# Kernel optimization log

Measured on AMD Instinct MI355X. Metric: run time of the kernel, lower is better.

## Reference

```python
import math
import jax, jax.numpy as jnp
import numpy as np

B, S, D, H, L, FF, V = 4, 512, 512, 8, 2, 2048, 32000
MAXSEQ = 1024
HD = D // H
SCALE = 1.0 / math.sqrt(HD)
EMB_SCALE = math.sqrt(D)


def _ln(x, w, b):
    m = x.mean(-1, keepdims=True)
    v = ((x - m) ** 2).mean(-1, keepdims=True)
    return (x - m) / jnp.sqrt(v + 1e-5) * w + b


def setup_inputs() -> dict:
    key = jax.random.key(0)
    ks = jax.random.split(key, 16)
    def n(i, shape):
        return 0.02 * jax.random.normal(ks[i], shape, dtype=jnp.float32)
    z = lambda shape: jnp.zeros(shape, dtype=jnp.float32)
    return {
        "input_ids": jax.random.randint(ks[0], (B, S), 0, V),
        "tok_emb": n(1, (V, D)),
        "pos_emb": n(2, (MAXSEQ, D)),
        "layer_weights": z((L + 1,)),
        "kW": n(3, (D, D)), "kb": z((D,)),
        "vW": n(4, (D, D)), "vb": z((D,)),
        "qW": n(5, (L, D, D)), "qb": z((L, D)),
        "oW": n(6, (L, D, D)), "ob": z((L, D)),
        "f1W": n(7, (L, D, FF)), "f1b": z((L, FF)),
        "f2W": n(8, (L, FF, D)), "f2b": z((L, D)),
        "ln1w": jnp.ones((L, D)), "ln1b": z((L, D)),
        "ln2w": jnp.ones((L, D)), "ln2b": z((L, D)),
        "lnfw": jnp.ones((D,)), "lnfb": z((D,)),
        "headW": n(9, (D, V)),
    }


def reference(input_ids, tok_emb, pos_emb, layer_weights, kW, kb, vW, vb,
              qW, qb, oW, ob, f1W, f1b, f2W, f2b,
              ln1w, ln1b, ln2w, ln2b, lnfw, lnfb, headW):
    # embeddings: (B,S,D)
    emb = tok_emb[input_ids] * EMB_SCALE + pos_emb[:S][None]
    w = jax.nn.softmax(layer_weights)  # (L+1,)

    def run_layers(x, mk, mv, mask):
        # x: (B,D); mk,mv: (B,M,D); mask: (M,) bool
        outs = [x]
        M = mk.shape[1]
        k = mk.reshape(B, M, H, HD)
        v = mv.reshape(B, M, H, HD)
        for l in range(L):
            q = (x @ qW[l] + qb[l]).reshape(B, H, HD)
            s = jnp.einsum('bhd,bmhd->bhm', q, k) * SCALE
            s = jnp.where(mask[None, None, :], s, -1e9)
            a = jax.nn.softmax(s, axis=-1)
            att = jnp.einsum('bhm,bmhd->bhd', a, v).reshape(B, D)
            att = att @ oW[l] + ob[l]
            x = _ln(x + att, ln1w[l], ln1b[l])
            ff = jax.nn.relu(x @ f1W[l] + f1b[l]) @ f2W[l] + f2b[l]
            x = _ln(x + ff, ln2w[l], ln2b[l])
            outs.append(x)
        return x, jnp.stack(outs, 0)  # (B,D), (L+1,B,D)

    # t = 0: no prior memory -> attend to K/V of the current embedding (mem_len=1)
    x0 = emb[:, 0]
    mk0 = (x0 @ kW + kb)[:, None, :]
    mv0 = (x0 @ vW + vb)[:, None, :]
    out0, louts0 = run_layers(x0, mk0, mv0, jnp.ones((1,), dtype=bool))
    m0 = jnp.einsum('l,lbd->bd', w, louts0)
    memk = jnp.zeros((B, S, D), dtype=emb.dtype).at[:, 0].set(m0 @ kW + kb)
    memv = jnp.zeros((B, S, D), dtype=emb.dtype).at[:, 0].set(m0 @ vW + vb)

    pos = jnp.arange(S)

    def step(carry, inputs):
        mk, mv = carry
        t, x = inputs  # t scalar int, x: (B,D)
        mask = pos < t  # valid memory slots: m_0..m_{t-1}
        out, louts = run_layers(x, mk, mv, mask)
        m = jnp.einsum('l,lbd->bd', w, louts)
        mk = mk.at[:, t].set(m @ kW + kb)
        mv = mv.at[:, t].set(m @ vW + vb)
        return (mk, mv), out

    ts = jnp.arange(1, S)
    xs_in = emb[:, 1:].transpose(1, 0, 2)  # (S-1,B,D)
    _, outs = jax.lax.scan(step, (memk, memv), (ts, xs_in))
    hidden = jnp.concatenate([out0[None], outs], axis=0).transpose(1, 0, 2)  # (B,S,D)
    hidden = _ln(hidden, lnfw, lnfb)
    return hidden @ headW  # (B,S,V)
```

## Files before the change

### kernel.cpp

```cpp
#include <hip/hip_runtime.h>
#include <hip/hip_cooperative_groups.h>
#include <math.h>

namespace cg = cooperative_groups;

#define NB 4
#define NS 512
#define ND 512
#define NH 8
#define NHD 64
#define NL 2
#define NFF 2048
#define NV 32000
#define ATT_SCALE 0.125f
#define EMB_SCALEF 22.627416997969522f

struct P {
  const int* ids;
  const float *tok, *pos, *lw, *kW, *kb, *vW, *vb, *qW, *qb, *oW, *ob;
  const float *f1W, *f1b, *f2W, *f2b, *ln1w, *ln1b, *ln2w, *ln2b, *lnfw, *lnfb, *headW;
  float *emb, *memk, *memv, *hidden, *q, *att, *r1, *r2, *ff1, *kv0k, *kv0v;
};

__device__ __forceinline__ float blk_sum(float v, float* red) {
  #pragma unroll
  for (int o = 32; o > 0; o >>= 1) v += __shfl_down(v, o, 64);
  const int tid = threadIdx.x;
  __syncthreads();
  if ((tid & 63) == 0) red[tid >> 6] = v;
  __syncthreads();
  return red[0] + red[1] + red[2] + red[3];
}

__device__ __forceinline__ float blk_max(float v, float* red) {
  #pragma unroll
  for (int o = 32; o > 0; o >>= 1) v = fmaxf(v, __shfl_down(v, o, 64));
  const int tid = threadIdx.x;
  __syncthreads();
  if ((tid & 63) == 0) red[tid >> 6] = v;
  __syncthreads();
  return fmaxf(fmaxf(red[0], red[1]), fmaxf(red[2], red[3]));
}

__device__ __forceinline__ void ln_stats(const float* __restrict__ v, float& mean, float& rstd, float* red) {
  const int tid = threadIdx.x;
  float s = 0.f, q = 0.f;
  for (int i = tid; i < ND; i += 256) { float x = v[i]; s += x; q += x * x; }
  s = blk_sum(s, red);
  q = blk_sum(q, red);
  mean = s * (1.0f / ND);
  rstd = rsqrtf(q * (1.0f / ND) - mean * mean + 1e-5f);
}

__global__ void __launch_bounds__(256) scan_kernel(P p) {
  cg::grid_group grid = cg::this_grid();
  const int wg = blockIdx.x;
  const int b = wg >> 4;
  const int sl = wg & 15;
  const int tid = threadIdx.x;

  __shared__ float xs[2048];
  __shared__ float part[256];
  __shared__ float red[4];

  for (int i = wg * 256 + tid; i < NB * NS * ND; i += 64 * 256) {
    int d = i & (ND - 1);
    int bs = i >> 9;
    int t = bs & (NS - 1);
    int bb = bs >> 9;
    p.emb[i] = p.tok[(size_t)p.ids[bb * NS + t] * ND + d] * EMB_SCALEF + p.pos[t * ND + d];
  }
  grid.sync();

  {
    for (int i = tid; i < ND; i += 256) xs[i] = p.emb[(size_t)b * NS * ND + i];
    __syncthreads();
    int oid = tid & 63, chunk = tid >> 6;
    bool isv = oid >= 32;
    int j = sl * 32 + (oid & 31);
    const float* W = isv ? p.vW : p.kW;
    const float* wp = W + (size_t)(chunk * 128) * ND + j;
    float acc = 0.f;
    #pragma unroll 4
    for (int d = 0; d < 128; d++) acc = fmaf(xs[chunk * 128 + d], wp[(size_t)d * ND], acc);
    part[tid] = acc;
    __syncthreads();
    if (tid < 64) {
      float r = part[tid] + part[64 + tid] + part[128 + tid] + part[192 + tid];
      bool iv = tid >= 32;
      int jj = sl * 32 + (tid & 31);
      if (!iv) p.kv0k[b * ND + jj] = r + p.kb[jj];
      else     p.kv0v[b * ND + jj] = r + p.vb[jj];
    }
  }
  grid.sync();

  float w0, w1, w2;
  {
    float a0 = p.lw[0], a1 = p.lw[1], a2 = p.lw[2];
    float mx = fmaxf(a0, fmaxf(a1, a2));
    float e0 = expf(a0 - mx), e1 = expf(a1 - mx), e2 = expf(a2 - mx);
    float inv = 1.f / (e0 + e1 + e2);
    w0 = e0 * inv; w1 = e1 * inv; w2 = e2 * inv;
  }

  for (int t = 0; t < NS; t++) {
    const float* xin0 = p.emb + ((size_t)b * NS + t) * ND;
    const int len = (t == 0) ? 1 : t;

    for (int l = 0; l < NL; l++) {
      if (l == 0) {
        for (int i = tid; i < ND; i += 256) xs[i] = xin0[i];
        __syncthreads();
      } else {
        const float* rv = p.r2 + (size_t)b * ND;
        float mean, rstd;
        ln_stats(rv, mean, rstd, red);
        for (int i = tid; i < ND; i += 256)
          xs[i] = (rv[i] - mean) * rstd * p.ln2w[i] + p.ln2b[i];
        __syncthreads();
      }
      {
        int jl = tid & 31, chunk = tid >> 5;
        int j = sl * 32 + jl;
        const float* wp = p.qW + (size_t)l * ND * ND + (size_t)(chunk * 64) * ND + j;
        float acc = 0.f;
        #pragma unroll 4
        for (int d = 0; d < 64; d++) acc = fmaf(xs[chunk * 64 + d], wp[(size_t)d * ND], acc);
        part[tid] = acc;
        __syncthreads();
        if (tid < 32) {
          float r = 0.f;
          #pragma unroll
          for (int c = 0; c < 8; c++) r += part[c * 32 + tid];
          int j2 = sl * 32 + tid;
          p.q[b * ND + j2] = r + p.qb[l * ND + j2];
        }
      }
      grid.sync();

      if (wg < 32) {
        int ab = wg >> 3, ah = wg & 7;
        const float* kp = (t == 0) ? (p.kv0k + ab * ND) : (p.memk + (size_t)ab * NS * ND);
        const float* vp = (t == 0) ? (p.kv0v + ab * ND) : (p.memv + (size_t)ab * NS * ND);
        if (tid < 64) xs[512 + tid] = p.q[ab * ND + ah * NHD + tid];
        __syncthreads();
        float lmax = -1e30f;
        for (int m = tid; m < len; m += 256) {
          const float* kr = kp + (size_t)m * ND + ah * NHD;
          float acc = 0.f;
          #pragma unroll
          for (int i = 0; i < NHD; i++) acc = fmaf(xs[512 + i], kr[i], acc);
          float sv = acc * ATT_SCALE;
          xs[m] = sv;
          lmax = fmaxf(lmax, sv);
        }
        lmax = blk_max(lmax, red);
        float lsum = 0.f;
        for (int m = tid; m < len; m += 256) { float e = expf(xs[m] - lmax); xs[m] = e; lsum += e; }
        lsum = blk_sum(lsum, red);
        float inv = 1.f / lsum;
        int hd = tid & 63, ch = tid >> 6;
        float acc = 0.f;
        for (int m = ch; m < len; m += 4) acc = fmaf(xs[m], vp[(size_t)m * ND + ah * NHD + hd], acc);
        part[tid] = acc;
        __syncthreads();
        if (tid < 64) {
          float r = (part[tid] + part[64 + tid] + part[128 + tid] + part[192 + tid]) * inv;
          p.att[ab * ND + ah * NHD + tid] = r;
        }
      }
      grid.sync();

      {
        for (int i = tid; i < ND; i += 256) xs[i] = p.att[b * ND + i];
        float mean = 0.f, rstd = 0.f;
        if (l == 1) {
          const float* rv = p.r2 + (size_t)b * ND;
          ln_stats(rv, mean, rstd, red);
        }
        __syncthreads();
        int jl = tid & 31, chunk = tid >> 5;
        int j = sl * 32 + jl;
        const float* wp = p.oW + (size_t)l * ND * ND + (size_t)(chunk * 64) * ND + j;
        float acc = 0.f;
        #pragma unroll 4
        for (int d = 0; d < 64; d++) acc = fmaf(xs[chunk * 64 + d], wp[(size_t)d * ND], acc);
        part[tid] = acc;
        __syncthreads();
        if (tid < 32) {
          float r = 0.f;
          #pragma unroll
          for (int c = 0; c < 8; c++) r += part[c * 32 + tid];
          int j2 = sl * 32 + tid;
          float xinv;
          if (l == 0) xinv = xin0[j2];
          else {
            const float* rv = p.r2 + (size_t)b * ND;
            xinv = (rv[j2] - mean) * rstd * p.ln2w[j2] + p.ln2b[j2];
          }
          p.r1[b * ND + j2] = xinv + r + p.ob[l * ND + j2];
        }
      }
      grid.sync();

      {
        const float* rv = p.r1 + b * ND;
        float mean, rstd;
        ln_stats(rv, mean, rstd, red);
        for (int i = tid; i < ND; i += 256)
          xs[i] = (rv[i] - mean) * rstd * p.ln1w[l * ND + i] + p.ln1b[l * ND + i];
        __syncthreads();
        int jl = tid & 127, chunk = tid >> 7;
        int j = sl * 128 + jl;
        const float* wp = p.f1W + (size_t)l * ND * NFF + (size_t)(chunk * 256) * NFF + j;
        float acc = 0.f;
        #pragma unroll 4
        for (int d = 0; d < 256; d++) acc = fmaf(xs[chunk * 256 + d], wp[(size_t)d * NFF], acc);
        part[tid] = acc;
        __syncthreads();
        if (tid < 128) {
          float r = part[tid] + part[128 + tid] + p.f1b[l * NFF + sl * 128 + tid];
          p.ff1[b * NFF + sl * 128 + tid] = fmaxf(r, 0.f);
        }
      }
      grid.sync();

      {
        for (int i = tid; i < NFF; i += 256) xs[i] = p.ff1[b * NFF + i];
        const float* rv = p.r1 + b * ND;
        float mean, rstd;
        ln_stats(rv, mean, rstd, red);
        __syncthreads();
        int jl = tid & 31, chunk = tid >> 5;
        int j = sl * 32 + jl;
        const float* wp = p.f2W + (size_t)l * NFF * ND + (size_t)(chunk * 256) * ND + j;
        float acc = 0.f;
        #pragma unroll 4
        for (int d = 0; d < 256; d++) acc = fmaf(xs[chunk * 256 + d], wp[(size_t)d * ND], acc);
        part[tid] = acc;
        __syncthreads();
        if (tid < 32) {
          float r = 0.f;
          #pragma unroll
          for (int c = 0; c < 8; c++) r += part[c * 32 + tid];
          int j2 = sl * 32 + tid;
          float x1 = (rv[j2] - mean) * rstd * p.ln1w[l * ND + j2] + p.ln1b[l * ND + j2];
          p.r2[((size_t)l * NB + b) * ND + j2] = x1 + r + p.f2b[l * ND + j2];
        }
      }
      grid.sync();
    }

    {
      const float* r20 = p.r2 + (size_t)b * ND;
      const float* r21 = p.r2 + ((size_t)NB + b) * ND;
      float m0, s0, m1, s1;
      ln_stats(r20, m0, s0, red);
      ln_stats(r21, m1, s1, red);
      for (int i = tid; i < ND; i += 256) {
        float x2 = (r20[i] - m0) * s0 * p.ln2w[i] + p.ln2b[i];
        float x4 = (r21[i] - m1) * s1 * p.ln2w[ND + i] + p.ln2b[ND + i];
        xs[i] = w0 * xin0[i] + w1 * x2 + w2 * x4;
        if (sl == 0) p.hidden[((size_t)b * NS + t) * ND + i] = x4;
      }
      __syncthreads();
      int oid = tid & 63, chunk = tid >> 6;
      bool isv = oid >= 32;
      int j = sl * 32 + (oid & 31);
      const float* W = isv ? p.vW : p.kW;
      const float* wp = W + (size_t)(chunk * 128) * ND + j;
      float acc = 0.f;
      #pragma unroll 4
      for (int d = 0; d < 128; d++) acc = fmaf(xs[chunk * 128 + d], wp[(size_t)d * ND], acc);
      part[tid] = acc;
      __syncthreads();
      if (tid < 64) {
        float r = part[tid] + part[64 + tid] + part[128 + tid] + part[192 + tid];
        bool iv = tid >= 32;
        int jj = sl * 32 + (tid & 31);
        if (!iv) p.memk[((size_t)b * NS + t) * ND + jj] = r + p.kb[jj];
        else     p.memv[((size_t)b * NS + t) * ND + jj] = r + p.vb[jj];
      }
    }
    grid.sync();
  }
}

__global__ void __launch_bounds__(256) lnf_kernel(const float* __restrict__ hidden,
                                                  const float* __restrict__ w,
                                                  const float* __restrict__ bi,
                                                  float* __restrict__ out) {
  __shared__ float red[4];
  const int row = blockIdx.x;
  const float* x = hidden + (size_t)row * ND;
  float mean, rstd;
  ln_stats(x, mean, rstd, red);
  for (int i = threadIdx.x; i < ND; i += 256)
    out[(size_t)row * ND + i] = (x[i] - mean) * rstd * w[i] + bi[i];
}

__global__ void __launch_bounds__(256) head_gemm(const float* __restrict__ A,
                                                 const float* __restrict__ Bw,
                                                 float* __restrict__ C) {
  __shared__ float As[8][128];
  __shared__ float Bs[8][128];
  const int tid = threadIdx.x;
  const int col0 = blockIdx.x * 128;
  const int row0 = blockIdx.y * 128;
  const int tx = tid & 15, ty = tid >> 4;
  float acc[8][8] = {};

  for (int k0 = 0; k0 < 512; k0 += 8) {
    {
      int r = tid >> 1, kk = (tid & 1) * 4;
      const float4 v = *(const float4*)(A + (size_t)(row0 + r) * 512 + k0 + kk);
      As[kk + 0][r] = v.x; As[kk + 1][r] = v.y; As[kk + 2][r] = v.z; As[kk + 3][r] = v.w;
      int brr = tid >> 5, bcc = (tid & 31) * 4;
      *(float4*)&Bs[brr][bcc] = *(const float4*)(Bw + (size_t)(k0 + brr) * NV + col0 + bcc);
    }
    __syncthreads();
    #pragma unroll
    for (int kk = 0; kk < 8; kk++) {
      float a[8], bv[8];
      #pragma unroll
      for (int i = 0; i < 8; i++) a[i] = As[kk][ty * 8 + i];
      #pragma unroll
      for (int j = 0; j < 8; j++) bv[j] = Bs[kk][tx * 8 + j];
      #pragma unroll
      for (int i = 0; i < 8; i++)
        #pragma unroll
        for (int j = 0; j < 8; j++) acc[i][j] = fmaf(a[i], bv[j], acc[i][j]);
    }
    __syncthreads();
  }
  #pragma unroll
  for (int i = 0; i < 8; i++) {
    float* cp = C + (size_t)(row0 + ty * 8 + i) * NV + col0 + tx * 8;
    float4 v0 = {acc[i][0], acc[i][1], acc[i][2], acc[i][3]};
    float4 v1 = {acc[i][4], acc[i][5], acc[i][6], acc[i][7]};
    *(float4*)cp = v0;
    *(float4*)(cp + 4) = v1;
  }
}

extern "C" void kernel_launch(void* const* d_in, const int* in_sizes, int n_in,
                              void* d_out, int out_size, void* d_ws, size_t ws_size,
                              hipStream_t stream) {
  P p;
  p.ids  = (const int*)d_in[0];
  p.tok  = (const float*)d_in[1];
  p.pos  = (const float*)d_in[2];
  p.lw   = (const float*)d_in[3];
  p.kW   = (const float*)d_in[4];
  p.kb   = (const float*)d_in[5];
  p.vW   = (const float*)d_in[6];
  p.vb   = (const float*)d_in[7];
  p.qW   = (const float*)d_in[8];
  p.qb   = (const float*)d_in[9];
  p.oW   = (const float*)d_in[10];
  p.ob   = (const float*)d_in[11];
  p.f1W  = (const float*)d_in[12];
  p.f1b  = (const float*)d_in[13];
  p.f2W  = (const float*)d_in[14];
  p.f2b  = (const float*)d_in[15];
  p.ln1w = (const float*)d_in[16];
  p.ln1b = (const float*)d_in[17];
  p.ln2w = (const float*)d_in[18];
  p.ln2b = (const float*)d_in[19];
  p.lnfw = (const float*)d_in[20];
  p.lnfb = (const float*)d_in[21];
  p.headW = (const float*)d_in[22];

  float* ws = (float*)d_ws;
  p.emb    = ws + 0;
  p.memk   = ws + 1048576;
  p.memv   = ws + 2097152;
  p.hidden = ws + 3145728;
  p.q      = ws + 4194304;
  p.att    = ws + 4196352;
  p.r1     = ws + 4198400;
  p.r2     = ws + 4200448;
  p.ff1    = ws + 4204544;
  p.kv0k   = ws + 4212736;
  p.kv0v   = ws + 4214784;

  void* args[] = { &p };
  hipLaunchCooperativeKernel((void*)scan_kernel, dim3(64), dim3(256), args, 0, stream);

  lnf_kernel<<<dim3(NB * NS), dim3(256), 0, stream>>>(p.hidden, p.lnfw, p.lnfb, p.emb);
  head_gemm<<<dim3(NV / 128, (NB * NS) / 128), dim3(256), 0, stream>>>(p.emb, p.headW, (float*)d_out);
}
```

Measured before the change: 92.25 ms.

## Rewrite scan kernel with 256 workgroups, LDS-resident weights, custom grid barrier

The persistent scan kernel grows from 64 to 256 workgroups, and each workgroup keeps its column slices of oW, f1W, f2W and kW/vW in LDS for the whole run, so those weights are no longer streamed from global memory every step. The layer-0 query projection is precomputed for all timesteps before the scan, pre-scaled. Attention is split four ways over memory slots and merged with a max/sum combine. cooperative-groups grid.sync is replaced by a hand-written hierarchical atomic barrier. The aim is to cut per-step weight traffic and sync latency, at the cost of heavy LDS use, one workgroup per CU, and a spin-wait barrier that relies on every workgroup being co-resident.

```diff
diff --git a/kernel.cpp b/kernel.cpp
--- a/kernel.cpp
+++ b/kernel.cpp
@@ -1,8 +1,5 @@
 #include <hip/hip_runtime.h>
-#include <hip/hip_cooperative_groups.h>
 #include <math.h>
-
-namespace cg = cooperative_groups;
 
 #define NB 4
 #define NS 512
@@ -12,15 +9,42 @@
 #define NL 2
 #define NFF 2048
 #define NV 32000
+#define NWG 256
 #define ATT_SCALE 0.125f
 #define EMB_SCALEF 22.627416997969522f
+
+#define OW_OFF 0
+#define OW_SZ  (2*2*513)
+#define F1_OFF (OW_OFF + OW_SZ)
+#define F1_SZ  (2*8*520)
+#define F2_OFF (F1_OFF + F1_SZ)
+#define F2_SZ  (2*2*2049)
+#define KV_OFF (F2_OFF + F2_SZ)
+#define KV_SZ  (4*513)
+#define W_TOTAL (KV_OFF + KV_SZ)
 
 struct P {
   const int* ids;
   const float *tok, *pos, *lw, *kW, *kb, *vW, *vb, *qW, *qb, *oW, *ob;
   const float *f1W, *f1b, *f2W, *f2b, *ln1w, *ln1b, *ln2w, *ln2b, *lnfw, *lnfb, *headW;
-  float *emb, *memk, *memv, *hidden, *q, *att, *r1, *r2, *ff1, *kv0k, *kv0v;
+  float *emb, *memk, *memv, *X, *r1g, *r2g, *ff1g, *attM, *attS, *attO, *kv0k, *kv0v;
+  int* bar;
 };
+
+__device__ __forceinline__ void gbar(int* bar, int iter) {
+  __syncthreads();
+  if (threadIdx.x == 0) {
+    __threadfence();
+    int li = blockIdx.x & 7;
+    int old = __hip_atomic_fetch_add(&bar[li * 32], 1, __ATOMIC_ACQ_REL, __HIP_MEMORY_SCOPE_AGENT);
+    if (old == iter * 32 + 31)
+      __hip_atomic_fetch_add(&bar[256], 1, __ATOMIC_ACQ_REL, __HIP_MEMORY_SCOPE_AGENT);
+    while (__hip_atomic_load(&bar[256], __ATOMIC_ACQUIRE, __HIP_MEMORY_SCOPE_AGENT) < iter * 8 + 8) {}
+    __threadfence();
+  }
+  __syncthreads();
+}
+#define GBAR() { gbar(p.bar, bar_iter); bar_iter++; }
 
 __device__ __forceinline__ float blk_sum(float v, float* red) {
   #pragma unroll
@@ -31,7 +55,6 @@
   __syncthreads();
   return red[0] + red[1] + red[2] + red[3];
 }
-
 __device__ __forceinline__ float blk_max(float v, float* red) {
   #pragma unroll
   for (int o = 32; o > 0; o >>= 1) v = fmaxf(v, __shfl_down(v, o, 64));
@@ -42,58 +65,91 @@
   return fmaxf(fmaxf(red[0], red[1]), fmaxf(red[2], red[3]));
 }
 
-__device__ __forceinline__ void ln_stats(const float* __restrict__ v, float& mean, float& rstd, float* red) {
+__global__ void __launch_bounds__(256, 1) scan_kernel(P p) {
+  const int wg = blockIdx.x;
   const int tid = threadIdx.x;
-  float s = 0.f, q = 0.f;
-  for (int i = tid; i < ND; i += 256) { float x = v[i]; s += x; q += x * x; }
-  s = blk_sum(s, red);
-  q = blk_sum(q, red);
-  mean = s * (1.0f / ND);
-  rstd = rsqrtf(q * (1.0f / ND) - mean * mean + 1e-5f);
-}
-
-__global__ void __launch_bounds__(256) scan_kernel(P p) {
-  cg::grid_group grid = cg::this_grid();
-  const int wg = blockIdx.x;
-  const int b = wg >> 4;
-  const int sl = wg & 15;
-  const int tid = threadIdx.x;
-
-  __shared__ float xs[2048];
+  __shared__ float wds[W_TOTAL];
+  __shared__ float xbuf[4 * 2064];
   __shared__ float part[256];
+  __shared__ float sc[256];
+  __shared__ float fct[128];
+  __shared__ float qv[64];
   __shared__ float red[4];
-
-  for (int i = wg * 256 + tid; i < NB * NS * ND; i += 64 * 256) {
-    int d = i & (ND - 1);
-    int bs = i >> 9;
-    int t = bs & (NS - 1);
-    int bb = bs >> 9;
-    p.emb[i] = p.tok[(size_t)p.ids[bb * NS + t] * ND + d] * EMB_SCALEF + p.pos[t * ND + d];
-  }
-  grid.sync();
+  __shared__ float stm[4], str[4], stm2[4], str2[4], stm3[4], str3[4];
+  int bar_iter = 0;
+
+  for (int e = tid; e < 2 * 2 * 512; e += 256) {
+    int k = e & 511, c = (e >> 9) & 1, l = e >> 10;
+    wds[OW_OFF + (l * 2 + c) * 513 + k] = p.oW[((size_t)l * ND + k) * ND + wg * 2 + c];
+  }
+  for (int e = tid; e < 2 * 512 * 8; e += 256) {
+    int c = e & 7, k = (e >> 3) & 511, l = e >> 12;
+    wds[F1_OFF + (l * 8 + c) * 520 + k] = p.f1W[((size_t)l * ND + k) * NFF + wg * 8 + c];
+  }
+  for (int e = tid; e < 2 * 2048 * 2; e += 256) {
+    int c = e & 1, k = (e >> 1) & 2047, l = e >> 12;
+    wds[F2_OFF + (l * 2 + c) * 2049 + k] = p.f2W[((size_t)l * NFF + k) * ND + wg * 2 + c];
+  }
+  for (int e = tid; e < 512 * 4; e += 256) {
+    int c = e & 3, k = e >> 2;
+    const float* W = (c < 2) ? p.kW : p.vW;
+    wds[KV_OFF + c * 513 + k] = W[(size_t)k * ND + wg * 2 + (c & 1)];
+  }
+  for (int i = wg * 256 + tid; i < NB * NS * ND; i += NWG * 256) {
+    int d = i & 511, bs = i >> 9, t = bs & 511, b = bs >> 9;
+    p.emb[i] = p.tok[(size_t)p.ids[b * NS + t] * ND + d] * EMB_SCALEF + p.pos[t * ND + d];
+  }
+  GBAR();
 
   {
-    for (int i = tid; i < ND; i += 256) xs[i] = p.emb[(size_t)b * NS * ND + i];
+    for (int pass = 0; pass < 2; pass++) {
+      int r0 = wg * 8 + pass * 4;
+      for (int v = tid; v < 4 * 512; v += 256) {
+        int rr = v >> 9, k = v & 511;
+        xbuf[rr * 516 + k] = p.emb[(size_t)(r0 + rr) * ND + k];
+      }
+      __syncthreads();
+      int j = tid;
+      float a0_[4] = {0, 0, 0, 0}, a1_[4] = {0, 0, 0, 0};
+      for (int k = 0; k < 512; k++) {
+        float w0v = p.qW[(size_t)k * ND + j];
+        float w1v = p.qW[(size_t)k * ND + j + 256];
+        #pragma unroll
+        for (int r = 0; r < 4; r++) {
+          float xv = xbuf[r * 516 + k];
+          a0_[r] = fmaf(xv, w0v, a0_[r]);
+          a1_[r] = fmaf(xv, w1v, a1_[r]);
+        }
+      }
+      float qb0 = p.qb[j], qb1 = p.qb[j + 256];
+      #pragma unroll
+      for (int r = 0; r < 4; r++) {
+        p.X[(size_t)(r0 + r) * ND + j] = (a0_[r] + qb0) * ATT_SCALE;
+        p.X[(size_t)(r0 + r) * ND + j + 256] = (a1_[r] + qb1) * ATT_SCALE;
+      }
+      __syncthreads();
+    }
+    for (int v = tid; v < 4 * 512; v += 256) {
+      int b = v >> 9, k = v & 511;
+      xbuf[b * 516 + k] = p.emb[((size_t)b * NS) * ND + k];
+    }
     __syncthreads();
-    int oid = tid & 63, chunk = tid >> 6;
-    bool isv = oid >= 32;
-    int j = sl * 32 + (oid & 31);
-    const float* W = isv ? p.vW : p.kW;
-    const float* wp = W + (size_t)(chunk * 128) * ND + j;
-    float acc = 0.f;
-    #pragma unroll 4
-    for (int d = 0; d < 128; d++) acc = fmaf(xs[chunk * 128 + d], wp[(size_t)d * ND], acc);
-    part[tid] = acc;
-    __syncthreads();
-    if (tid < 64) {
-      float r = part[tid] + part[64 + tid] + part[128 + tid] + part[192 + tid];
-      bool iv = tid >= 32;
-      int jj = sl * 32 + (tid & 31);
-      if (!iv) p.kv0k[b * ND + jj] = r + p.kb[jj];
-      else     p.kv0v[b * ND + jj] = r + p.vb[jj];
-    }
-  }
-  grid.sync();
+    {
+      int kc = tid & 15, dot = tid >> 4, c = dot & 3, b = dot >> 2;
+      const float* wcol = &wds[KV_OFF + c * 513];
+      float acc = 0.f;
+      #pragma unroll 8
+      for (int k = kc; k < 512; k += 16) acc = fmaf(xbuf[b * 516 + k], wcol[k], acc);
+      #pragma unroll
+      for (int o = 8; o; o >>= 1) acc += __shfl_down(acc, o, 16);
+      if (kc == 0) {
+        int j = wg * 2 + (c & 1);
+        if (c < 2) p.kv0k[b * ND + j] = acc + p.kb[j];
+        else       p.kv0v[b * ND + j] = acc + p.vb[j];
+      }
+    }
+  }
+  GBAR();
 
   float w0, w1, w2;
   {
@@ -105,185 +161,219 @@
   }
 
   for (int t = 0; t < NS; t++) {
-    const float* xin0 = p.emb + ((size_t)b * NS + t) * ND;
     const int len = (t == 0) ? 1 : t;
 
     for (int l = 0; l < NL; l++) {
-      if (l == 0) {
-        for (int i = tid; i < ND; i += 256) xs[i] = xin0[i];
-        __syncthreads();
-      } else {
-        const float* rv = p.r2 + (size_t)b * ND;
-        float mean, rstd;
-        ln_stats(rv, mean, rstd, red);
-        for (int i = tid; i < ND; i += 256)
-          xs[i] = (rv[i] - mean) * rstd * p.ln2w[i] + p.ln2b[i];
-        __syncthreads();
-      }
-      {
-        int jl = tid & 31, chunk = tid >> 5;
-        int j = sl * 32 + jl;
-        const float* wp = p.qW + (size_t)l * ND * ND + (size_t)(chunk * 64) * ND + j;
-        float acc = 0.f;
-        #pragma unroll 4
-        for (int d = 0; d < 64; d++) acc = fmaf(xs[chunk * 64 + d], wp[(size_t)d * ND], acc);
-        part[tid] = acc;
-        __syncthreads();
-        if (tid < 32) {
-          float r = 0.f;
-          #pragma unroll
-          for (int c = 0; c < 8; c++) r += part[c * 32 + tid];
-          int j2 = sl * 32 + tid;
-          p.q[b * ND + j2] = r + p.qb[l * ND + j2];
-        }
-      }
-      grid.sync();
-
-      if (wg < 32) {
-        int ab = wg >> 3, ah = wg & 7;
-        const float* kp = (t == 0) ? (p.kv0k + ab * ND) : (p.memk + (size_t)ab * NS * ND);
-        const float* vp = (t == 0) ? (p.kv0v + ab * ND) : (p.memv + (size_t)ab * NS * ND);
-        if (tid < 64) xs[512 + tid] = p.q[ab * ND + ah * NHD + tid];
-        __syncthreads();
-        float lmax = -1e30f;
-        for (int m = tid; m < len; m += 256) {
-          const float* kr = kp + (size_t)m * ND + ah * NHD;
+      if (wg < 128) {
+        const int b = wg >> 5, h = (wg >> 2) & 7, qd = wg & 3;
+        const int len4 = (len + 3) >> 2;
+        const int lo = qd * len4;
+        const int hi = min(lo + len4, len);
+        const int cnt = hi - lo;
+
+        if (l == 0) {
+          if (tid < 64) qv[tid] = p.X[((size_t)b * NS + t) * ND + h * 64 + tid];
+          __syncthreads();
+        } else {
+          float s = 0.f, q = 0.f;
+          for (int i = tid; i < 512; i += 256) { float x = p.r2g[b * ND + i]; s += x; q += x * x; }
+          s = blk_sum(s, red); q = blk_sum(q, red);
+          float mean = s * (1.f / 512), rstd = rsqrtf(q * (1.f / 512) - mean * mean + 1e-5f);
+          for (int i = tid; i < 512; i += 256)
+            xbuf[i] = (p.r2g[b * ND + i] - mean) * rstd * p.ln2w[i] + p.ln2b[i];
+          __syncthreads();
+          {
+            int d = tid & 63, kc = tid >> 6;
+            const float* wq = p.qW + (size_t)ND * ND;
+            float acc = 0.f;
+            for (int k = kc; k < 512; k += 4)
+              acc = fmaf(xbuf[k], wq[(size_t)k * ND + h * 64 + d], acc);
+            part[tid] = acc;
+            __syncthreads();
+            if (tid < 64)
+              qv[tid] = (part[tid] + part[64 + tid] + part[128 + tid] + part[192 + tid]
+                         + p.qb[ND + h * 64 + tid]) * ATT_SCALE;
+            __syncthreads();
+          }
+        }
+        const float* kbase = (t == 0) ? (p.kv0k + b * ND) : (p.memk + (size_t)b * NS * ND);
+        const float* vbase = (t == 0) ? (p.kv0v + b * ND) : (p.memv + (size_t)b * NS * ND);
+        float s = -1e30f;
+        if (tid < cnt) {
+          int m = lo + tid;
+          const float4* kr4 = (const float4*)(kbase + (size_t)m * ND + h * 64);
           float acc = 0.f;
           #pragma unroll
-          for (int i = 0; i < NHD; i++) acc = fmaf(xs[512 + i], kr[i], acc);
-          float sv = acc * ATT_SCALE;
-          xs[m] = sv;
-          lmax = fmaxf(lmax, sv);
-        }
-        lmax = blk_max(lmax, red);
-        float lsum = 0.f;
-        for (int m = tid; m < len; m += 256) { float e = expf(xs[m] - lmax); xs[m] = e; lsum += e; }
-        lsum = blk_sum(lsum, red);
-        float inv = 1.f / lsum;
-        int hd = tid & 63, ch = tid >> 6;
+          for (int i = 0; i < 16; i++) {
+            float4 kv4 = kr4[i];
+            acc = fmaf(qv[i * 4 + 0], kv4.x, acc);
+            acc = fmaf(qv[i * 4 + 1], kv4.y, acc);
+            acc = fmaf(qv[i * 4 + 2], kv4.z, acc);
+            acc = fmaf(qv[i * 4 + 3], kv4.w, acc);
+          }
+          s = acc;
+        }
+        float M = blk_max(s, red);
+        float e = (tid < cnt) ? __expf(s - M) : 0.f;
+        sc[tid] = e;
+        float S = blk_sum(e, red);
+        {
+          int d = tid & 63, mc = tid >> 6;
+          float acc = 0.f;
+          for (int m = lo + mc; m < hi; m += 4)
+            acc = fmaf(sc[m - lo], vbase[(size_t)m * ND + h * 64 + d], acc);
+          part[tid] = acc;
+          __syncthreads();
+          if (tid < 64)
+            p.attO[((b * 8 + h) * 4 + qd) * 64 + tid] =
+                part[tid] + part[64 + tid] + part[128 + tid] + part[192 + tid];
+          if (tid == 0) { p.attM[(b * 8 + h) * 4 + qd] = M; p.attS[(b * 8 + h) * 4 + qd] = S; }
+        }
+      }
+      GBAR();
+
+      {
+        if (tid < 32) {
+          float M0 = p.attM[tid * 4 + 0], M1 = p.attM[tid * 4 + 1];
+          float M2 = p.attM[tid * 4 + 2], M3 = p.attM[tid * 4 + 3];
+          float M = fmaxf(fmaxf(M0, M1), fmaxf(M2, M3));
+          float e0 = __expf(M0 - M), e1 = __expf(M1 - M), e2 = __expf(M2 - M), e3 = __expf(M3 - M);
+          float den = e0 * p.attS[tid * 4 + 0] + e1 * p.attS[tid * 4 + 1]
+                    + e2 * p.attS[tid * 4 + 2] + e3 * p.attS[tid * 4 + 3];
+          float inv = 1.f / den;
+          fct[tid * 4 + 0] = e0 * inv; fct[tid * 4 + 1] = e1 * inv;
+          fct[tid * 4 + 2] = e2 * inv; fct[tid * 4 + 3] = e3 * inv;
+        }
+        if (l == 1) {
+          int wv = tid >> 6, lane = tid & 63;
+          float s = 0.f, q = 0.f;
+          for (int i = lane; i < 512; i += 64) { float x = p.r2g[wv * ND + i]; s += x; q += x * x; }
+          #pragma unroll
+          for (int o = 32; o; o >>= 1) { s += __shfl_down(s, o, 64); q += __shfl_down(q, o, 64); }
+          if (lane == 0) {
+            float mean = s * (1.f / 512);
+            stm2[wv] = mean; str2[wv] = rsqrtf(q * (1.f / 512) - mean * mean + 1e-5f);
+          }
+        }
+        __syncthreads();
+        for (int v = tid; v < 2048; v += 256) {
+          int b = v >> 9, j = v & 511, h = j >> 6, d = j & 63;
+          int bh = b * 8 + h;
+          float a = fct[bh * 4 + 0] * p.attO[(bh * 4 + 0) * 64 + d]
+                  + fct[bh * 4 + 1] * p.attO[(bh * 4 + 1) * 64 + d]
+                  + fct[bh * 4 + 2] * p.attO[(bh * 4 + 2) * 64 + d]
+                  + fct[bh * 4 + 3] * p.attO[(bh * 4 + 3) * 64 + d];
+          xbuf[b * 516 + j] = a;
+        }
+        __syncthreads();
+        int kc = tid & 31, dot = tid >> 5, c = dot & 1, b = dot >> 1;
+        const float* wcol = &wds[OW_OFF + (l * 2 + c) * 513];
         float acc = 0.f;
-        for (int m = ch; m < len; m += 4) acc = fmaf(xs[m], vp[(size_t)m * ND + ah * NHD + hd], acc);
-        part[tid] = acc;
+        #pragma unroll 8
+        for (int k = kc; k < 512; k += 32) acc = fmaf(xbuf[b * 516 + k], wcol[k], acc);
+        #pragma unroll
+        for (int o = 16; o; o >>= 1) acc += __shfl_down(acc, o, 32);
+        if (kc == 0) {
+          int j = wg * 2 + c;
+          float resid;
+          if (l == 0) resid = p.emb[((size_t)b * NS + t) * ND + j];
+          else        resid = (p.r2g[b * ND + j] - stm2[b]) * str2[b] * p.ln2w[j] + p.ln2b[j];
+          p.r1g[(l * NB + b) * ND + j] = resid + acc + p.ob[l * ND + j];
+        }
+      }
+      GBAR();
+
+      {
+        int wv = tid >> 6, lane = tid & 63;
+        float s = 0.f, q = 0.f;
+        for (int i = lane; i < 512; i += 64) { float x = p.r1g[(l * NB + wv) * ND + i]; s += x; q += x * x; }
+        #pragma unroll
+        for (int o = 32; o; o >>= 1) { s += __shfl_down(s, o, 64); q += __shfl_down(q, o, 64); }
+        if (lane == 0) {
+          float mean = s * (1.f / 512);
+          stm[wv] = mean; str[wv] = rsqrtf(q * (1.f / 512) - mean * mean + 1e-5f);
+        }
         __syncthreads();
-        if (tid < 64) {
-          float r = (part[tid] + part[64 + tid] + part[128 + tid] + part[192 + tid]) * inv;
-          p.att[ab * ND + ah * NHD + tid] = r;
-        }
-      }
-      grid.sync();
+        for (int v = tid; v < 2048; v += 256) {
+          int b = v >> 9, i = v & 511;
+          xbuf[b * 516 + i] = (p.r1g[(l * NB + b) * ND + i] - stm[b]) * str[b]
+                              * p.ln1w[l * ND + i] + p.ln1b[l * ND + i];
+        }
+        __syncthreads();
+        int kc = tid & 7, dot = tid >> 3, c = dot & 7, b = dot >> 3;
+        const float* wcol = &wds[F1_OFF + (l * 8 + c) * 520];
+        float acc = 0.f;
+        #pragma unroll 8
+        for (int k = kc; k < 512; k += 8) acc = fmaf(xbuf[b * 516 + k], wcol[k], acc);
+        #pragma unroll
+        for (int o = 4; o; o >>= 1) acc += __shfl_down(acc, o, 8);
+        if (kc == 0) {
+          int j = wg * 8 + c;
+          p.ff1g[b * NFF + j] = fmaxf(acc + p.f1b[l * NFF + j], 0.f);
+        }
+      }
+      GBAR();
 
       {
-        for (int i = tid; i < ND; i += 256) xs[i] = p.att[b * ND + i];
-        float mean = 0.f, rstd = 0.f;
-        if (l == 1) {
-          const float* rv = p.r2 + (size_t)b * ND;
-          ln_stats(rv, mean, rstd, red);
+        for (int v = tid; v < 4 * 2048; v += 256) {
+          int b = v >> 11, k = v & 2047;
+          xbuf[b * 2064 + k] = p.ff1g[b * NFF + k];
         }
         __syncthreads();
-        int jl = tid & 31, chunk = tid >> 5;
-        int j = sl * 32 + jl;
-        const float* wp = p.oW + (size_t)l * ND * ND + (size_t)(chunk * 64) * ND + j;
+        int kc = tid & 31, dot = tid >> 5, c = dot & 1, b = dot >> 1;
+        const float* wcol = &wds[F2_OFF + (l * 2 + c) * 2049];
         float acc = 0.f;
-        #pragma unroll 4
-        for (int d = 0; d < 64; d++) acc = fmaf(xs[chunk * 64 + d], wp[(size_t)d * ND], acc);
-        part[tid] = acc;
-        __syncthreads();
-        if (tid < 32) {
-          float r = 0.f;
-          #pragma unroll
-          for (int c = 0; c < 8; c++) r += part[c * 32 + tid];
-          int j2 = sl * 32 + tid;
-          float xinv;
-          if (l == 0) xinv = xin0[j2];
-          else {
-            const float* rv = p.r2 + (size_t)b * ND;
-            xinv = (rv[j2] - mean) * rstd * p.ln2w[j2] + p.ln2b[j2];
-          }
-          p.r1[b * ND + j2] = xinv + r + p.ob[l * ND + j2];
-        }
-      }
-      grid.sync();
-
-      {
-        const float* rv = p.r1 + b * ND;
-        float mean, rstd;
-        ln_stats(rv, mean, rstd, red);
-        for (int i = tid; i < ND; i += 256)
-          xs[i] = (rv[i] - mean) * rstd * p.ln1w[l * ND + i] + p.ln1b[l * ND + i];
-        __syncthreads();
-        int jl = tid & 127, chunk = tid >> 7;
-        int j = sl * 128 + jl;
-        const float* wp = p.f1W + (size_t)l * ND * NFF + (size_t)(chunk * 256) * NFF + j;
-        float acc = 0.f;
-        #pragma unroll 4
-        for (int d = 0; d < 256; d++) acc = fmaf(xs[chunk * 256 + d], wp[(size_t)d * NFF], acc);
-        part[tid] = acc;
-        __syncthreads();
-        if (tid < 128) {
-          float r = part[tid] + part[128 + tid] + p.f1b[l * NFF + sl * 128 + tid];
-          p.ff1[b * NFF + sl * 128 + tid] = fmaxf(r, 0.f);
-        }
-      }
-      grid.sync();
-
-      {
-        for (int i = tid; i < NFF; i += 256) xs[i] = p.ff1[b * NFF + i];
-        const float* rv = p.r1 + b * ND;
-        float mean, rstd;
-        ln_stats(rv, mean, rstd, red);
-        __syncthreads();
-        int jl = tid & 31, chunk = tid >> 5;
-        int j = sl * 32 + jl;
-        const float* wp = p.f2W + (size_t)l * NFF * ND + (size_t)(chunk * 256) * ND + j;
-        float acc = 0.f;
-        #pragma unroll 4
-        for (int d = 0; d < 256; d++) acc = fmaf(xs[chunk * 256 + d], wp[(size_t)d * ND], acc);
-        part[tid] = acc;
-        __syncthreads();
-        if (tid < 32) {
-          float r = 0.f;
-          #pragma unroll
-          for (int c = 0; c < 8; c++) r += part[c * 32 + tid];
-          int j2 = sl * 32 + tid;
-          float x1 = (rv[j2] - mean) * rstd * p.ln1w[l * ND + j2] + p.ln1b[l * ND + j2];
-          p.r2[((size_t)l * NB + b) * ND + j2] = x1 + r + p.f2b[l * ND + j2];
-        }
-      }
-      grid.sync();
+        #pragma unroll 8
+        for (int k = kc; k < 2048; k += 32) acc = fmaf(xbuf[b * 2064 + k], wcol[k], acc);
+        #pragma unroll
+        for (int o = 16; o; o >>= 1) acc += __shfl_down(acc, o, 32);
+        if (kc == 0) {
+          int j = wg * 2 + c;
+          float x1 = (p.r1g[(l * NB + b) * ND + j] - stm[b]) * str[b]
+                     * p.ln1w[l * ND + j] + p.ln1b[l * ND + j];
+          p.r2g[(l * NB + b) * ND + j] = x1 + acc + p.f2b[l * ND + j];
+        }
+      }
+      GBAR();
     }
 
     {
-      const float* r20 = p.r2 + (size_t)b * ND;
-      const float* r21 = p.r2 + ((size_t)NB + b) * ND;
-      float m0, s0, m1, s1;
-      ln_stats(r20, m0, s0, red);
-      ln_stats(r21, m1, s1, red);
-      for (int i = tid; i < ND; i += 256) {
-        float x2 = (r20[i] - m0) * s0 * p.ln2w[i] + p.ln2b[i];
-        float x4 = (r21[i] - m1) * s1 * p.ln2w[ND + i] + p.ln2b[ND + i];
-        xs[i] = w0 * xin0[i] + w1 * x2 + w2 * x4;
-        if (sl == 0) p.hidden[((size_t)b * NS + t) * ND + i] = x4;
+      int wv = tid >> 6, lane = tid & 63;
+      for (int pass = 0; pass < 2; pass++) {
+        float s = 0.f, q = 0.f;
+        for (int i = lane; i < 512; i += 64) { float x = p.r2g[(pass * NB + wv) * ND + i]; s += x; q += x * x; }
+        #pragma unroll
+        for (int o = 32; o; o >>= 1) { s += __shfl_down(s, o, 64); q += __shfl_down(q, o, 64); }
+        if (lane == 0) {
+          float mean = s * (1.f / 512), rstd = rsqrtf(q * (1.f / 512) - mean * mean + 1e-5f);
+          if (pass == 0) { stm2[wv] = mean; str2[wv] = rstd; }
+          else           { stm3[wv] = mean; str3[wv] = rstd; }
+        }
       }
       __syncthreads();
-      int oid = tid & 63, chunk = tid >> 6;
-      bool isv = oid >= 32;
-      int j = sl * 32 + (oid & 31);
-      const float* W = isv ? p.vW : p.kW;
-      const float* wp = W + (size_t)(chunk * 128) * ND + j;
+      for (int v = tid; v < 2048; v += 256) {
+        int b = v >> 9, j = v & 511;
+        float e = p.emb[((size_t)b * NS + t) * ND + j];
+        float x20 = (p.r2g[b * ND + j] - stm2[b]) * str2[b] * p.ln2w[j] + p.ln2b[j];
+        float x21 = (p.r2g[(NB + b) * ND + j] - stm3[b]) * str3[b] * p.ln2w[ND + j] + p.ln2b[ND + j];
+        xbuf[b * 516 + j] = w0 * e + w1 * x20 + w2 * x21;
+        if (wg == b) p.X[((size_t)b * NS + t) * ND + j] = x21;
+      }
+      __syncthreads();
+      int kc = tid & 15, dot = tid >> 4, c = dot & 3, b = dot >> 2;
+      const float* wcol = &wds[KV_OFF + c * 513];
       float acc = 0.f;
-      #pragma unroll 4
-      for (int d = 0; d < 128; d++) acc = fmaf(xs[chunk * 128 + d], wp[(size_t)d * ND], acc);
-      part[tid] = acc;
-      __syncthreads();
-      if (tid < 64) {
-        float r = part[tid] + part[64 + tid] + part[128 + tid] + part[192 + tid];
-        bool iv = tid >= 32;
-        int jj = sl * 32 + (tid & 31);
-        if (!iv) p.memk[((size_t)b * NS + t) * ND + jj] = r + p.kb[jj];
-        else     p.memv[((size_t)b * NS + t) * ND + jj] = r + p.vb[jj];
-      }
-    }
-    grid.sync();
+      #pragma unroll 8
+      for (int k = kc; k < 512; k += 16) acc = fmaf(xbuf[b * 516 + k], wcol[k], acc);
+      #pragma unroll
+      for (int o = 8; o; o >>= 1) acc += __shfl_down(acc, o, 16);
+      if (kc == 0) {
+        int j = wg * 2 + (c & 1);
+        if (c < 2) p.memk[((size_t)b * NS + t) * ND + j] = acc + p.kb[j];
+        else       p.memv[((size_t)b * NS + t) * ND + j] = acc + p.vb[j];
+      }
+    }
+    GBAR();
   }
 }
 
@@ -294,9 +384,14 @@
   __shared__ float red[4];
   const int row = blockIdx.x;
   const float* x = hidden + (size_t)row * ND;
-  float mean, rstd;
-  ln_stats(x, mean, rstd, red);
-  for (int i = threadIdx.x; i < ND; i += 256)
+  const int tid = threadIdx.x;
+  float s = 0.f, q = 0.f;
+  for (int i = tid; i < ND; i += 256) { float v = x[i]; s += v; q += v * v; }
+  s = blk_sum(s, red);
+  q = blk_sum(q, red);
+  float mean = s * (1.0f / ND);
+  float rstd = rsqrtf(q * (1.0f / ND) - mean * mean + 1e-5f);
+  for (int i = tid; i < ND; i += 256)
     out[(size_t)row * ND + i] = (x[i] - mean) * rstd * w[i] + bi[i];
 }
 
@@ -373,21 +468,25 @@
   p.headW = (const float*)d_in[22];
 
   float* ws = (float*)d_ws;
-  p.emb    = ws + 0;
-  p.memk   = ws + 1048576;
-  p.memv   = ws + 2097152;
-  p.hidden = ws + 3145728;
-  p.q      = ws + 4194304;
-  p.att    = ws + 4196352;
-  p.r1     = ws + 4198400;
-  p.r2     = ws + 4200448;
-  p.ff1    = ws + 4204544;
-  p.kv0k   = ws + 4212736;
-  p.kv0v   = ws + 4214784;
-
+  p.emb  = ws;
+  p.memk = ws + 1048576;
+  p.memv = ws + 2097152;
+  p.X    = ws + 3145728;
+  float* base = ws + 4194304;
+  p.kv0k = base;  base += 2048;
+  p.kv0v = base;  base += 2048;
+  p.r1g  = base;  base += 4096;
+  p.r2g  = base;  base += 4096;
+  p.ff1g = base;  base += 8192;
+  p.attM = base;  base += 128;
+  p.attS = base;  base += 128;
+  p.attO = base;  base += 8192;
+  p.bar  = (int*)base;
+
+  hipMemsetAsync(p.bar, 0, 512 * sizeof(int), stream);
   void* args[] = { &p };
-  hipLaunchCooperativeKernel((void*)scan_kernel, dim3(64), dim3(256), args, 0, stream);
-
-  lnf_kernel<<<dim3(NB * NS), dim3(256), 0, stream>>>(p.hidden, p.lnfw, p.lnfb, p.emb);
+  hipLaunchCooperativeKernel((void*)scan_kernel, dim3(NWG), dim3(256), args, 0, stream);
+
+  lnf_kernel<<<dim3(NB * NS), dim3(256), 0, stream>>>(p.X, p.lnfw, p.lnfb, p.emb);
   head_gemm<<<dim3(NV / 128, (NB * NS) / 128), dim3(256), 0, stream>>>(p.emb, p.headW, (float*)d_out);
 }
```

After: 162.0 ms. 75.6% more time.
